# Optimization experiments

Measured on AMD Instinct MI355X. Metric: run time of the kernel, lower is better.

Reference implementation:

```python
import jax, jax.numpy as jnp
import numpy as np

N = 8192
D = 768
TEMPERATURE = 0.1
EPS_NORM = 1e-8   # torch CosineSimilarity eps
EPS_LOG = 1e-6


def setup_inputs() -> dict:
    key = jax.random.key(0)
    k1, k2, k3 = jax.random.split(key, 3)
    features = jax.random.normal(k1, (N, D), dtype=jnp.float32)
    positive_mask = jax.random.randint(k2, (N, N), 0, 2).astype(jnp.float32)
    negative_mask = jax.random.randint(k3, (N, N), 0, 2).astype(jnp.float32)
    return {"features": features, "positive_mask": positive_mask, "negative_mask": negative_mask}


def reference(features, positive_mask, negative_mask):
    n = features.shape[0]
    # cosine similarity: normalize then GEMM (same math as broadcasted CosineSimilarity)
    norms = jnp.linalg.norm(features, axis=1, keepdims=True)
    fn = features / jnp.maximum(norms, EPS_NORM)
    sim = jnp.exp(jnp.matmul(fn, fn.T) / TEMPERATURE)  # [N, N]
    # zero out self-contrast on the diagonal of both masks
    not_eye = 1.0 - jnp.eye(n, dtype=features.dtype)
    pm = positive_mask * not_eye
    nm = negative_mask * not_eye
    pos_sums = pm.sum(axis=1)
    pos_sums = jnp.where(pos_sums == 0, 1.0, pos_sums)
    neg = jnp.sum(sim * nm, axis=1, keepdims=True)  # [N, 1]
    log_prob = -jnp.log(sim / neg + EPS_LOG)        # [N, N]
    per_row = jnp.sum(log_prob * pm, axis=1) / pos_sums
    return jnp.mean(per_row)
```

## Files before the change

### kernel.cpp

```cpp
#include <hip/hip_runtime.h>
#include <hip/hip_bf16.h>

#define NROWS 8192
#define DDIM 768

typedef short short8 __attribute__((ext_vector_type(8)));
typedef float floatx4 __attribute__((ext_vector_type(4)));
typedef float f4 __attribute__((ext_vector_type(4)));
#define TSTRIDE2 260

#define SLB(k) (((k) * 128) / 24)

__global__ __launch_bounds__(256) void normalize_k(const float* __restrict__ f,
                                                   __hip_bfloat16* __restrict__ fn) {
    const int row = blockIdx.x;
    const int t = threadIdx.x;
    const float* fr = f + (size_t)row * DDIM;
    float v0 = fr[t];
    float v1 = fr[t + 256];
    float v2 = fr[t + 512];
    float ss = v0 * v0 + v1 * v1 + v2 * v2;
#pragma unroll
    for (int m = 32; m; m >>= 1) ss += __shfl_xor(ss, m, 64);
    __shared__ float wsum[4];
    if ((t & 63) == 0) wsum[t >> 6] = ss;
    __syncthreads();
    float tot = wsum[0] + wsum[1] + wsum[2] + wsum[3];
    float inv = 1.0f / fmaxf(sqrtf(tot), 1e-8f);
    __hip_bfloat16* o = fn + (size_t)row * DDIM;
    o[t]       = __float2bfloat16(v0 * inv);
    o[t + 256] = __float2bfloat16(v1 * inv);
    o[t + 512] = __float2bfloat16(v2 * inv);
}

__global__ __launch_bounds__(512, 2) void ntxent_main(
        const __hip_bfloat16* __restrict__ fn,
        const float* __restrict__ pmask, const float* __restrict__ nmask,
        float* __restrict__ negG, float* __restrict__ sG,
        float* __restrict__ pG) {
    __shared__ __align__(16) char smem[131072];
    char* IsB = smem;
    char* JsB = smem + 16384;
    char* maskLds = smem + 32768;
    float* T = (float*)smem;

    const int t = threadIdx.x;
    const int lane = t & 63;
    const int wv = t >> 6;
    const int wn = wv & 1;
    const int wm = wv >> 1;
    const int q  = lane >> 4;
    const int cl = lane & 15;

    const int bt0 = blockIdx.x;
    const int bt = (bt0 & 7) * 66 + (bt0 >> 3);

    int r = (int)((sqrtf(8.0f * (float)bt + 1.0f) - 1.0f) * 0.5f);
    while ((r + 1) * (r + 2) / 2 <= bt) ++r;
    while (r * (r + 1) / 2 > bt) --r;
    const int c = bt - r * (r + 1) / 2;
    const int rowBase = c * 256;
    const int colBase = r * 256;
    const bool offDiag = (c != r);

    const int rdSw = ((q ^ ((cl >> 1) & 3)) << 4);

    const int sRow = t >> 6;
    const int sChunk = (t & 63) ^ (sRow & 7);

    floatx4 acc[4][8];
#pragma unroll
    for (int mf = 0; mf < 4; ++mf)
#pragma unroll
        for (int nf = 0; nf < 8; ++nf)
            acc[mf][nf] = (floatx4){0.f, 0.f, 0.f, 0.f};

    unsigned int dw[8] = {0u,0u,0u,0u,0u,0u,0u,0u};
    unsigned int mw[8] = {0u,0u,0u,0u,0u,0u,0u,0u};

    auto issue_slab = [&](int s) {
        const int slot = s % 12;
        const int side = s >> 6;
        const int rg   = (s & 63) >> 1;
        const float* mp = (s & 1) ? nmask : pmask;
        const int rowG = (side ? colBase : rowBase) + rg * 8 + sRow;
        const int colG = (side ? rowBase : colBase) + sChunk * 4;
        const float* src = mp + (size_t)rowG * NROWS + colG;
        __builtin_amdgcn_global_load_lds(
            (const __attribute__((address_space(1))) void*)src,
            (__attribute__((address_space(3))) void*)(maskLds + slot * 8192 + t * 16),
            16, 0, 0);
    };

    auto issue_fn = [&](int k0) {
#pragma unroll
        for (int it = 0; it < 2; ++it) {
            const int s = it * 512 + t;
            const int rr = s >> 2;
            const int cg = (s & 3) ^ ((rr >> 1) & 3);
            const __hip_bfloat16* ga = fn + (size_t)(rowBase + rr) * DDIM + k0 + cg * 8;
            const __hip_bfloat16* gb = fn + (size_t)(colBase + rr) * DDIM + k0 + cg * 8;
            __builtin_amdgcn_global_load_lds(
                (const __attribute__((address_space(1))) void*)ga,
                (__attribute__((address_space(3))) void*)(IsB + s * 16), 16, 0, 0);
            __builtin_amdgcn_global_load_lds(
                (const __attribute__((address_space(1))) void*)gb,
                (__attribute__((address_space(3))) void*)(JsB + s * 16), 16, 0, 0);
        }
    };

    auto pack_slab = [&](int s) {
        const int slot = s % 12;
        const int side = s >> 6;
        const int rg   = (s & 63) >> 1;
        const int sh   = (s & 1) ? 16 : 0;
        if (side == 0) {
            if (wn == ((rg >> 4) & 1) && (cl >> 3) == (rg & 1)) {
                const int nf = (rg >> 1) & 7;
                const int rl = cl & 7;
                const char* base = maskLds + slot * 8192 + rl * 1024;
                float word = 0.f;
#pragma unroll
                for (int mf = 3; mf >= 0; --mf) {
                    const int pos = (wm * 16 + mf * 4 + q) ^ rl;
                    const f4 m = *(const f4*)(base + pos * 16);
                    float nib = fmaf(2.f, m[1], m[0]) + fmaf(8.f, m[3], 4.f * m[2]);
                    word = fmaf(word, 16.f, nib);
                }
                dw[nf] |= ((unsigned int)word) << sh;
            }
        } else if (offDiag) {
            if ((t >> 7) == (rg & 3)) {
                const int st = rg >> 2;
                const int rl = (t >> 4) & 7;
                const char* base = maskLds + slot * 8192 + rl * 1024;
                float word = 0.f;
#pragma unroll
                for (int u = 3; u >= 0; --u) {
                    const int pos = ((t & 15) * 4 + u) ^ rl;
                    const f4 m = *(const f4*)(base + pos * 16);
                    float nib = fmaf(2.f, m[1], m[0]) + fmaf(8.f, m[3], 4.f * m[2]);
                    word = fmaf(word, 16.f, nib);
                }
                mw[st] |= ((unsigned int)word) << sh;
            }
        }
    };

#pragma unroll
    for (int s = 0; s < SLB(1); ++s) issue_slab(s);

#pragma unroll
    for (int kt = 0; kt < 24; ++kt) {
        asm volatile("s_waitcnt lgkmcnt(0)\n\ts_barrier" ::: "memory");

        issue_fn(kt * 32);

#pragma unroll
        for (int gl = 0; gl < 6; ++gl) {
            const int s = SLB(kt + 1) + gl;
            if (s < SLB(kt + 2)) issue_slab(s);
        }

#pragma unroll
        for (int gl = 0; gl < 6; ++gl) {
            const int s = SLB(kt) + gl;
            if (s < SLB(kt + 1)) pack_slab(s);
        }

        if (kt == 23)           asm volatile("s_waitcnt vmcnt(0)\n\ts_barrier" ::: "memory");
        else if ((kt % 3) == 1) asm volatile("s_waitcnt vmcnt(6)\n\ts_barrier" ::: "memory");
        else                    asm volatile("s_waitcnt vmcnt(5)\n\ts_barrier" ::: "memory");

#pragma unroll
        for (int h = 0; h < 2; ++h) {
            short8 if_[4];
#pragma unroll
            for (int nf = 0; nf < 4; ++nf) {
                const int rr = wn * 128 + (h * 4 + nf) * 16 + cl;
                if_[nf] = *(const short8*)(IsB + rr * 64 + rdSw);
            }
#pragma unroll
            for (int mf = 0; mf < 4; ++mf) {
                const int rr = wm * 64 + mf * 16 + cl;
                const short8 jf = *(const short8*)(JsB + rr * 64 + rdSw);
#pragma unroll
                for (int nf = 0; nf < 4; ++nf)
                    acc[mf][h * 4 + nf] = __builtin_amdgcn_mfma_f32_16x16x32_bf16(
                        jf, if_[nf], acc[mf][h * 4 + nf], 0, 0, 0);
            }
        }
    }

    const int jb0 = colBase + wm * 64 + q * 4;
#pragma unroll
    for (int nf = 0; nf < 8; ++nf) {
        const int grow = rowBase + wn * 128 + nf * 16 + cl;
        const unsigned int w = dw[nf];
        float aN = 0.f, aS = 0.f, aP = 0.f;
#pragma unroll
        for (int mf = 0; mf < 4; ++mf) {
            const int jbase = jb0 + mf * 16;
#pragma unroll
            for (int reg = 0; reg < 4; ++reg) {
                const int b = mf * 4 + reg;
                float pmv = ((w >> b) & 1u) ? 1.0f : 0.0f;
                float nmv = ((w >> (16 + b)) & 1u) ? 1.0f : 0.0f;
                if (grow == jbase + reg) { pmv = 0.f; nmv = 0.f; }
                float v = acc[mf][nf][reg];
                float e = __builtin_amdgcn_exp2f(v * 14.4269504089f);
                aN = fmaf(nmv, e, aN);
                aS = fmaf(pmv, v, aS);
                aP += pmv;
            }
        }
        aN += __shfl_xor(aN, 16, 64);  aN += __shfl_xor(aN, 32, 64);
        aS += __shfl_xor(aS, 16, 64);  aS += __shfl_xor(aS, 32, 64);
        aP += __shfl_xor(aP, 16, 64);  aP += __shfl_xor(aP, 32, 64);
        if (q == 0) {
            atomicAdd(&negG[grow], aN);
            atomicAdd(&sG[grow],   aS);
            atomicAdd(&pG[grow],   aP);
        }
    }

    if (offDiag) {
        const int jl2 = t >> 4;
        const int iseg = (t & 15) * 16;
#pragma unroll
        for (int st = 0; st < 8; ++st) {
            __syncthreads();
            if (wm == (st >> 1)) {
#pragma unroll
                for (int m2 = 0; m2 < 2; ++m2) {
                    const int mf = (st & 1) * 2 + m2;
#pragma unroll
                    for (int nf = 0; nf < 8; ++nf) {
                        const int i = wn * 128 + nf * 16 + cl;
#pragma unroll
                        for (int reg = 0; reg < 4; ++reg) {
                            const int jl = m2 * 16 + q * 4 + reg;
                            T[jl * TSTRIDE2 + i] = acc[mf][nf][reg];
                        }
                    }
                }
            }
            __syncthreads();
            const int jg = colBase + st * 32 + jl2;
            const unsigned int w = mw[st];
            const f4* tv = (const f4*)(T + jl2 * TSTRIDE2 + iseg);
            float aN = 0.f, aS = 0.f, aP = 0.f;
#pragma unroll
            for (int u = 0; u < 4; ++u) {
                f4 v4 = tv[u];
#pragma unroll
                for (int e = 0; e < 4; ++e) {
                    const int b = u * 4 + e;
                    float v = v4[e];
                    float pmv = ((w >> b) & 1u) ? 1.0f : 0.0f;
                    float nmv = ((w >> (16 + b)) & 1u) ? 1.0f : 0.0f;
                    float ex = __builtin_amdgcn_exp2f(v * 14.4269504089f);
                    aN = fmaf(nmv, ex, aN);
                    aS = fmaf(pmv, v, aS);
                    aP += pmv;
                }
            }
            aN += __shfl_xor(aN, 1, 64); aN += __shfl_xor(aN, 2, 64);
            aN += __shfl_xor(aN, 4, 64); aN += __shfl_xor(aN, 8, 64);
            aS += __shfl_xor(aS, 1, 64); aS += __shfl_xor(aS, 2, 64);
            aS += __shfl_xor(aS, 4, 64); aS += __shfl_xor(aS, 8, 64);
            aP += __shfl_xor(aP, 1, 64); aP += __shfl_xor(aP, 2, 64);
            aP += __shfl_xor(aP, 4, 64); aP += __shfl_xor(aP, 8, 64);
            if ((t & 15) == 0) {
                atomicAdd(&negG[jg], aN);
                atomicAdd(&sG[jg],   aS);
                atomicAdd(&pG[jg],   aP);
            }
        }
    }
}

__global__ __launch_bounds__(1024) void final_k(const float* __restrict__ negG,
        const float* __restrict__ sG, const float* __restrict__ pG,
        float* __restrict__ out) {
    const int t = threadIdx.x;
    float sum = 0.f;
    for (int i = t; i < NROWS; i += 1024) {
        float P = pG[i];
        if (P > 0.f) {
            sum += (P * logf(negG[i]) - 10.0f * sG[i]) / P;
        }
    }
#pragma unroll
    for (int m = 32; m; m >>= 1) sum += __shfl_xor(sum, m, 64);
    __shared__ float wsum[16];
    if ((t & 63) == 0) wsum[t >> 6] = sum;
    __syncthreads();
    if (t < 16) {
        float v = wsum[t];
#pragma unroll
        for (int m = 8; m; m >>= 1) v += __shfl_xor(v, m, 16);
        if (t == 0) out[0] = v / (float)NROWS;
    }
}

extern "C" void kernel_launch(void* const* d_in, const int* in_sizes, int n_in,
                              void* d_out, int out_size, void* d_ws, size_t ws_size,
                              hipStream_t stream) {
    const float* feat  = (const float*)d_in[0];
    const float* pmask = (const float*)d_in[1];
    const float* nmask = (const float*)d_in[2];
    float* out = (float*)d_out;

    char* ws = (char*)d_ws;
    __hip_bfloat16* fn = (__hip_bfloat16*)ws;
    float* negG = (float*)(ws + 12582912);
    float* sG = negG + NROWS;
    float* pG = sG + NROWS;

    hipMemsetAsync(negG, 0, 3 * NROWS * sizeof(float), stream);

    normalize_k<<<NROWS, 256, 0, stream>>>(feat, fn);

    ntxent_main<<<528, 512, 0, stream>>>(fn, pmask, nmask, negG, sG, pG);

    final_k<<<1, 1024, 0, stream>>>(negG, sG, pG, out);
}
```

Baseline: 647.5 us.

## Double-buffer feature tiles in LDS and reorder mask slab issue/pack

Splits the shared memory into two 32 KB feature buffers so the next K-step's bf16 tiles are prefetched while the current step's MFMAs run, instead of loading and consuming the same buffer in one iteration. The mask ring shrinks from 12 slots to 8 to make room. Mask slab issue moves after packing, with an extra barrier. The MFMA inner loop is split into four halves with two B fragments each to reduce live fragment registers. This aims to hide global-to-LDS latency for the GEMM operands, at the cost of a smaller mask prefetch depth and more barriers.

```diff
diff --git a/kernel.cpp b/kernel.cpp
--- a/kernel.cpp
+++ b/kernel.cpp
@@ -39,9 +39,9 @@
         float* __restrict__ negG, float* __restrict__ sG,
         float* __restrict__ pG) {
     __shared__ __align__(16) char smem[131072];
-    char* IsB = smem;
-    char* JsB = smem + 16384;
-    char* maskLds = smem + 32768;
+    char* fnBuf0 = smem;
+    char* fnBuf1 = smem + 32768;
+    char* maskLds = smem + 65536;
     float* T = (float*)smem;
 
     const int t = threadIdx.x;
@@ -79,7 +79,7 @@
     unsigned int mw[8] = {0u,0u,0u,0u,0u,0u,0u,0u};
 
     auto issue_slab = [&](int s) {
-        const int slot = s % 12;
+        const int slot = s & 7;
         const int side = s >> 6;
         const int rg   = (s & 63) >> 1;
         const float* mp = (s & 1) ? nmask : pmask;
@@ -92,7 +92,7 @@
             16, 0, 0);
     };
 
-    auto issue_fn = [&](int k0) {
+    auto issue_fn = [&](char* buf, int k0) {
 #pragma unroll
         for (int it = 0; it < 2; ++it) {
             const int s = it * 512 + t;
@@ -102,15 +102,15 @@
             const __hip_bfloat16* gb = fn + (size_t)(colBase + rr) * DDIM + k0 + cg * 8;
             __builtin_amdgcn_global_load_lds(
                 (const __attribute__((address_space(1))) void*)ga,
-                (__attribute__((address_space(3))) void*)(IsB + s * 16), 16, 0, 0);
+                (__attribute__((address_space(3))) void*)(buf + s * 16), 16, 0, 0);
             __builtin_amdgcn_global_load_lds(
                 (const __attribute__((address_space(1))) void*)gb,
-                (__attribute__((address_space(3))) void*)(JsB + s * 16), 16, 0, 0);
+                (__attribute__((address_space(3))) void*)(buf + 16384 + s * 16), 16, 0, 0);
         }
     };
 
     auto pack_slab = [&](int s) {
-        const int slot = s % 12;
+        const int slot = s & 7;
         const int side = s >> 6;
         const int rg   = (s & 63) >> 1;
         const int sh   = (s & 1) ? 16 : 0;
@@ -147,47 +147,53 @@
         }
     };
 
+    issue_fn(fnBuf0, 0);
 #pragma unroll
     for (int s = 0; s < SLB(1); ++s) issue_slab(s);
+    asm volatile("s_waitcnt vmcnt(0)" ::: "memory");
 
 #pragma unroll
     for (int kt = 0; kt < 24; ++kt) {
         asm volatile("s_waitcnt lgkmcnt(0)\n\ts_barrier" ::: "memory");
 
-        issue_fn(kt * 32);
-
-#pragma unroll
-        for (int gl = 0; gl < 6; ++gl) {
-            const int s = SLB(kt + 1) + gl;
-            if (s < SLB(kt + 2)) issue_slab(s);
-        }
+        if (kt < 23) issue_fn((kt & 1) ? fnBuf0 : fnBuf1, (kt + 1) * 32);
+
+        if (kt < 23) asm volatile("s_waitcnt vmcnt(4)\n\ts_barrier" ::: "memory");
+        else         asm volatile("s_waitcnt vmcnt(0)\n\ts_barrier" ::: "memory");
 
 #pragma unroll
         for (int gl = 0; gl < 6; ++gl) {
             const int s = SLB(kt) + gl;
             if (s < SLB(kt + 1)) pack_slab(s);
         }
-
-        if (kt == 23)           asm volatile("s_waitcnt vmcnt(0)\n\ts_barrier" ::: "memory");
-        else if ((kt % 3) == 1) asm volatile("s_waitcnt vmcnt(6)\n\ts_barrier" ::: "memory");
-        else                    asm volatile("s_waitcnt vmcnt(5)\n\ts_barrier" ::: "memory");
-
-#pragma unroll
-        for (int h = 0; h < 2; ++h) {
-            short8 if_[4];
-#pragma unroll
-            for (int nf = 0; nf < 4; ++nf) {
-                const int rr = wn * 128 + (h * 4 + nf) * 16 + cl;
-                if_[nf] = *(const short8*)(IsB + rr * 64 + rdSw);
+        asm volatile("s_barrier" ::: "memory");
+
+        if (kt < 23) {
+#pragma unroll
+            for (int gl = 0; gl < 6; ++gl) {
+                const int s = SLB(kt + 1) + gl;
+                if (s < SLB(kt + 2)) issue_slab(s);
+            }
+        }
+
+        const char* IsC = (kt & 1) ? fnBuf1 : fnBuf0;
+        const char* JsC = IsC + 16384;
+#pragma unroll
+        for (int h = 0; h < 4; ++h) {
+            short8 if_[2];
+#pragma unroll
+            for (int nf = 0; nf < 2; ++nf) {
+                const int rr = wn * 128 + (h * 2 + nf) * 16 + cl;
+                if_[nf] = *(const short8*)(IsC + rr * 64 + rdSw);
             }
 #pragma unroll
             for (int mf = 0; mf < 4; ++mf) {
                 const int rr = wm * 64 + mf * 16 + cl;
-                const short8 jf = *(const short8*)(JsB + rr * 64 + rdSw);
-#pragma unroll
-                for (int nf = 0; nf < 4; ++nf)
-                    acc[mf][h * 4 + nf] = __builtin_amdgcn_mfma_f32_16x16x32_bf16(
-                        jf, if_[nf], acc[mf][h * 4 + nf], 0, 0, 0);
+                const short8 jf = *(const short8*)(JsC + rr * 64 + rdSw);
+#pragma unroll
+                for (int nf = 0; nf < 2; ++nf)
+                    acc[mf][h * 2 + nf] = __builtin_amdgcn_mfma_f32_16x16x32_bf16(
+                        jf, if_[nf], acc[mf][h * 2 + nf], 0, 0, 0);
             }
         }
     }
```

Result: faster. 616.0 us (-4.9%).
